# Performance work log

Measured on AMD Instinct MI355X. Metric: run time of the kernel, lower is better.

Reference implementation:

```python
import jax, jax.numpy as jnp
import numpy as np

L, B, T, C, H, FF = 2, 2, 2048, 512, 8, 1024
HS = C // H  # head size
EPS = 1.1920929e-07  # torch float32 finfo eps (nn.RMSNorm default)


def setup_inputs() -> dict:
    key = jax.random.key(0)
    ks = jax.random.split(key, 20)
    s = 0.02
    return {
        "hidden": jax.random.normal(ks[0], (B, T, C), jnp.float32),
        "target": jax.random.normal(ks[1], (B, T, C), jnp.float32),
        # self-attn per-head projections (bias=False)
        "Wq_s": jax.random.normal(ks[2], (L, H, C, HS)) * s,
        "Wk_s": jax.random.normal(ks[3], (L, H, C, HS)) * s,
        "Wv_s": jax.random.normal(ks[4], (L, H, C, HS)) * s,
        "Wo_s": jax.random.normal(ks[5], (L, C, C)) * s,
        "bo_s": jnp.zeros((L, C)),
        # cross-attn per-head projections
        "Wq_x": jax.random.normal(ks[6], (L, H, C, HS)) * s,
        "Wk_x": jax.random.normal(ks[7], (L, H, C, HS)) * s,
        "Wv_x": jax.random.normal(ks[8], (L, H, C, HS)) * s,
        "Wo_x": jax.random.normal(ks[9], (L, C, C)) * s,
        "bo_x": jnp.zeros((L, C)),
        # FFN
        "W1": jax.random.normal(ks[10], (L, C, FF)) * s,
        "b1": jnp.zeros((L, FF)),
        "W2": jax.random.normal(ks[11], (L, FF, C)) * s,
        "b2": jnp.zeros((L, C)),
        # RMSNorm gains ln1..ln4
        "g1": jnp.ones((L, C)),
        "g2": jnp.ones((L, C)),
        "g3": jnp.ones((L, C)),
        "g4": jnp.ones((L, C)),
    }


def _rms(x, g):
    return x * jax.lax.rsqrt(jnp.mean(x * x, axis=-1, keepdims=True) + EPS) * g


def _attn(q_in, kv_in, Wq, Wk, Wv, Wo, bo, causal):
    # q_in: [B,Tq,C], kv_in: [B,Tk,C]; W*: [H,C,HS]
    q = jnp.einsum('btc,hcd->bhtd', q_in, Wq)
    k = jnp.einsum('bsc,hcd->bhsd', kv_in, Wk)
    v = jnp.einsum('bsc,hcd->bhsd', kv_in, Wv)
    wei = jnp.einsum('bhtd,bhsd->bhts', q, k) * (HS ** -0.5)  # [B,H,Tq,Tk]
    if causal:
        Tq, Tk = q_in.shape[1], kv_in.shape[1]
        mask = jnp.tril(jnp.ones((Tq, Tk), bool))
        wei = jnp.where(mask, wei, -jnp.inf)
    wei = jax.nn.softmax(wei, axis=-1)
    out = jnp.einsum('bhts,bhsd->bhtd', wei, v)
    out = out.transpose(0, 2, 1, 3).reshape(q_in.shape[0], q_in.shape[1], C)
    return out @ Wo + bo


def reference(hidden, target, Wq_s, Wk_s, Wv_s, Wo_s, bo_s,
              Wq_x, Wk_x, Wv_x, Wo_x, bo_x,
              W1, b1, W2, b2, g1, g2, g3, g4):
    t = target
    for l in range(L):
        # masked self-attention with RMSNorm pre-norm + residual
        t = t + _attn(_rms(t, g1[l]), _rms(t, g1[l]), Wq_s[l], Wk_s[l], Wv_s[l],
                      Wo_s[l], bo_s[l], causal=True)
        # cross-attention: K/V from ln2(hidden), Q from ln3(t)
        t = t + _attn(_rms(t, g3[l]), _rms(hidden, g2[l]), Wq_x[l], Wk_x[l], Wv_x[l],
                      Wo_x[l], bo_x[l], causal=False)
        # GELU FFN
        h = _rms(t, g4[l])
        t = t + (jax.nn.gelu(h @ W1[l] + b1[l], approximate=False) @ W2[l] + b2[l])
    return t
```

## Files before the change

kernel.cpp:

```cpp
#include <hip/hip_runtime.h>
#include <hip/hip_bf16.h>
#include <math.h>

#define L 2
#define B 2
#define T 2048
#define C 512
#define H 8
#define FF 1024
#define HS 64
#define EPSV 1.1920929e-07f

typedef __hip_bfloat16 bf16;
typedef __attribute__((ext_vector_type(8))) short short8;
typedef __attribute__((ext_vector_type(4))) float f32x4;

__device__ __forceinline__ float b2f(bf16 x) { return __bfloat162float(x); }

__device__ __forceinline__ void gl16(const unsigned short* g, unsigned short* l) {
    __builtin_amdgcn_global_load_lds(
        (const __attribute__((address_space(1))) unsigned int*)g,
        (__attribute__((address_space(3))) unsigned int*)l, 16, 0, 0);
}

__global__ void detect_k(const unsigned short* __restrict__ g1bits, int* __restrict__ flag) {
    if (threadIdx.x == 0 && blockIdx.x == 0)
        *flag = (g1bits[0] != (unsigned short)0x3F80u) ? 1 : 0;
}

__device__ __forceinline__ float ld_in(const void* p, size_t i, int fl) {
    return fl ? ((const float*)p)[i] : b2f(((const bf16*)p)[i]);
}

#define QKVT_TOT 1572864
#define WO_TOT 524288
#define W12_TOT 1048576
#define SM_TOT 9216
#define ACT_TOT 2097152

struct TrArgs {
    const void *Wq_s, *Wk_s, *Wv_s, *Wq_x, *Wk_x, *Wv_x, *Wo_s, *Wo_x, *W1, *W2;
    bf16 *cQKVs, *cQKVx, *cWoTs, *cWoTx, *cW1T, *cW2T;
    const int* flag;
};

__global__ __launch_bounds__(256) void prep_tr_k(TrArgs a) {
    __shared__ float tile[32][33];
    int bid = blockIdx.x;
    int fl = *a.flag;
    const void* src; bf16* dst;
    size_t sbase;
    int srcLD, dstLD, r0, c0;
    if (bid < 3072) {
        int pid = bid >> 5, t = bid & 31;
        int which = pid / 48, rem = pid % 48;
        int l = rem / 24, rem2 = rem % 24;
        int p = rem2 >> 3, hh = rem2 & 7;
        src = which ? (p == 0 ? a.Wq_x : p == 1 ? a.Wk_x : a.Wv_x)
                    : (p == 0 ? a.Wq_s : p == 1 ? a.Wk_s : a.Wv_s);
        dst = (which ? a.cQKVx : a.cQKVs) + (size_t)l * 786432 + (size_t)(p * 512 + hh * 64) * 512;
        sbase = (size_t)(l * 8 + hh) * 32768;
        srcLD = 64; dstLD = 512;
        r0 = (t >> 1) * 32; c0 = (t & 1) * 32;
    } else if (bid < 4096) {
        int b2 = bid - 3072, pid = b2 >> 8, t = b2 & 255;
        int which = pid >> 1, l = pid & 1;
        src = which ? a.Wo_x : a.Wo_s;
        dst = (which ? a.cWoTx : a.cWoTs) + (size_t)l * 262144;
        sbase = (size_t)l * 262144;
        srcLD = 512; dstLD = 512;
        r0 = (t >> 4) * 32; c0 = (t & 15) * 32;
    } else if (bid < 5120) {
        int b2 = bid - 4096, l = b2 >> 9, t = b2 & 511;
        src = a.W1; dst = a.cW1T + (size_t)l * 524288; sbase = (size_t)l * 524288;
        srcLD = 1024; dstLD = 512;
        r0 = (t >> 5) * 32; c0 = (t & 31) * 32;
    } else {
        int b2 = bid - 5120, l = b2 >> 9, t = b2 & 511;
        src = a.W2; dst = a.cW2T + (size_t)l * 524288; sbase = (size_t)l * 524288;
        srcLD = 512; dstLD = 1024;
        r0 = (t >> 4) * 32; c0 = (t & 15) * 32;
    }
    int tx = threadIdx.x & 31, ty = threadIdx.x >> 5;
#pragma unroll
    for (int i = 0; i < 4; i++)
        tile[ty + i * 8][tx] = ld_in(src, sbase + (size_t)(r0 + ty + i * 8) * srcLD + c0 + tx, fl);
    __syncthreads();
#pragma unroll
    for (int i = 0; i < 4; i++)
        dst[(size_t)(c0 + ty + i * 8) * dstLD + r0 + tx] = __float2bfloat16(tile[tx][ty + i * 8]);
}

#define ACTQ 1048576
struct SmArgs {
    const void* sm[8];
    const void *hidden, *target;
    bf16* smallDst;
    float *hid, *t_buf;
    const int* flag;
};

__global__ void prep_small_k(SmArgs s) {
    int i = blockIdx.x * 256 + threadIdx.x;
    int fl = *s.flag;
    if (i < SM_TOT) {
        const int cum[9] = {0, 1024, 2048, 4096, 5120, 6144, 7168, 8192, 9216};
        int k = 0;
        while (i >= cum[k + 1]) k++;
        s.smallDst[i] = __float2bfloat16(ld_in(s.sm[k], i - cum[k], fl));
        return;
    }
    int q = i - SM_TOT;
    if (q >= ACTQ) return;
    int half = q >= (ACTQ / 2);
    size_t e = (size_t)(q - half * (ACTQ / 2)) * 4;
    const void* src = half ? s.target : s.hidden;
    float* dstf = half ? s.t_buf : s.hid;
    if (fl) {
        *(float4*)(dstf + e) = *(const float4*)((const float*)src + e);
    } else {
        ushort4 u = *(const ushort4*)((const unsigned short*)src + e);
        float4 v;
        v.x = __uint_as_float((unsigned)u.x << 16);
        v.y = __uint_as_float((unsigned)u.y << 16);
        v.z = __uint_as_float((unsigned)u.z << 16);
        v.w = __uint_as_float((unsigned)u.w << 16);
        *(float4*)(dstf + e) = v;
    }
}

__global__ void write_out_k(const float* __restrict__ in, void* __restrict__ out, int n,
                            const int* __restrict__ flag) {
    int i = blockIdx.x * blockDim.x + threadIdx.x;
    if (i >= n) return;
    if (*flag) ((float*)out)[i] = in[i];
    else       ((bf16*)out)[i] = __float2bfloat16(in[i]);
}

__global__ void rmsnorm_k(const float* __restrict__ x, const bf16* __restrict__ g,
                          bf16* __restrict__ y) {
    int row = blockIdx.x;
    int tid = threadIdx.x;
    const float* xr = x + (size_t)row * C;
    float v0 = xr[tid], v1 = xr[tid + 256];
    __shared__ float red[256];
    red[tid] = v0 * v0 + v1 * v1;
    __syncthreads();
    for (int s = 128; s > 0; s >>= 1) {
        if (tid < s) red[tid] += red[tid + s];
        __syncthreads();
    }
    float sc = rsqrtf(red[0] / (float)C + EPSV);
    y[(size_t)row * C + tid] = __float2bfloat16(v0 * sc * b2f(g[tid]));
    y[(size_t)row * C + tid + 256] = __float2bfloat16(v1 * sc * b2f(g[tid + 256]));
}

__global__ void rmsnorm2_k(const float* __restrict__ xa, const bf16* __restrict__ ga,
                           bf16* __restrict__ ya, const float* __restrict__ xb,
                           const bf16* __restrict__ gb, bf16* __restrict__ yb) {
    int sel = blockIdx.y;
    const float* x = sel ? xb : xa;
    const bf16* g = sel ? gb : ga;
    bf16* y = sel ? yb : ya;
    int row = blockIdx.x;
    int tid = threadIdx.x;
    const float* xr = x + (size_t)row * C;
    float v0 = xr[tid], v1 = xr[tid + 256];
    __shared__ float red[256];
    red[tid] = v0 * v0 + v1 * v1;
    __syncthreads();
    for (int s = 128; s > 0; s >>= 1) {
        if (tid < s) red[tid] += red[tid + s];
        __syncthreads();
    }
    float sc = rsqrtf(red[0] / (float)C + EPSV);
    y[(size_t)row * C + tid] = __float2bfloat16(v0 * sc * b2f(g[tid]));
    y[(size_t)row * C + tid + 256] = __float2bfloat16(v1 * sc * b2f(g[tid + 256]));
}

struct GDesc {
    const bf16* A; const bf16* Bt; const bf16* bias; float* resid; bf16* out;
    int N, K, ldOut, ep, nblkx, blkofs;
};
struct GBatch { GDesc d[3]; int nd; };

__global__ __launch_bounds__(256) void gemm64_k(GBatch gb) {
    int bid = blockIdx.x;
    int di = 0;
    if (gb.nd > 1 && bid >= gb.d[1].blkofs) di = 1;
    if (gb.nd > 2 && bid >= gb.d[2].blkofs) di = 2;
    GDesc g = gb.d[di];
    int lb = bid - g.blkofs;
    int bx = lb % g.nblkx, by = lb / g.nblkx;
    int m0 = by * 64, n0 = bx * 64;

    __shared__ alignas(16) unsigned short As[2][64 * 64];
    __shared__ alignas(16) unsigned short Bs[2][64 * 64];
    int tid = threadIdx.x, lane = tid & 63, wave = tid >> 6;
    int wr = wave >> 1, wc = wave & 1, quad = lane >> 4, l15 = lane & 15;
    const unsigned short* Au = (const unsigned short*)g.A;
    const unsigned short* Bu = (const unsigned short*)g.Bt;

    int r0 = tid >> 3, sg = tid & 7;
    int gs = sg ^ (r0 & 7);
    const unsigned short* agp0 = Au + (size_t)(m0 + r0) * g.K + gs * 8;
    const unsigned short* agp1 = Au + (size_t)(m0 + r0 + 32) * g.K + gs * 8;
    const unsigned short* bgp0 = Bu + (size_t)(n0 + r0) * g.K + gs * 8;
    const unsigned short* bgp1 = Bu + (size_t)(n0 + r0 + 32) * g.K + gs * 8;
    int wofs = wave * 512;

    f32x4 zf = {0.f, 0.f, 0.f, 0.f};
    f32x4 acc[2][2];
    acc[0][0] = zf; acc[0][1] = zf; acc[1][0] = zf; acc[1][1] = zf;

    int sws0 = ((quad) ^ (l15 & 7)) * 8;
    int sws1 = ((4 + quad) ^ (l15 & 7)) * 8;
    int arow = wr * 32 + l15, brow = wc * 32 + l15;

    int nk = g.K >> 6;
    {
        gl16(agp0, &As[0][wofs]);
        gl16(agp1, &As[0][wofs + 2048]);
        gl16(bgp0, &Bs[0][wofs]);
        gl16(bgp1, &Bs[0][wofs + 2048]);
    }
    int buf = 0;
    for (int kt = 0; kt < nk; kt++) {
        __builtin_amdgcn_sched_barrier(0);
        __builtin_amdgcn_s_barrier();
        __builtin_amdgcn_sched_barrier(0);
        if (kt + 1 < nk) {
            int ko = (kt + 1) << 6;
            gl16(agp0 + ko, &As[buf ^ 1][wofs]);
            gl16(agp1 + ko, &As[buf ^ 1][wofs + 2048]);
            gl16(bgp0 + ko, &Bs[buf ^ 1][wofs]);
            gl16(bgp1 + ko, &Bs[buf ^ 1][wofs + 2048]);
            asm volatile("s_waitcnt vmcnt(4)" ::: "memory");
        } else {
            asm volatile("s_waitcnt vmcnt(0)" ::: "memory");
        }
        __builtin_amdgcn_sched_barrier(0);
        __builtin_amdgcn_s_barrier();
        __builtin_amdgcn_sched_barrier(0);

        const unsigned short* Ab = As[buf];
        const unsigned short* Bb = Bs[buf];
        short8 a0[2], b0[2], a1[2], b1[2];
#pragma unroll
        for (int i = 0; i < 2; i++) {
            int ra = (arow + i * 16) << 6, rb = (brow + i * 16) << 6;
            a0[i] = *(const short8*)(Ab + ra + sws0);
            a1[i] = *(const short8*)(Ab + ra + sws1);
            b0[i] = *(const short8*)(Bb + rb + sws0);
            b1[i] = *(const short8*)(Bb + rb + sws1);
        }
#pragma unroll
        for (int mi = 0; mi < 2; mi++)
#pragma unroll
            for (int ni = 0; ni < 2; ni++) {
                acc[mi][ni] =
                    __builtin_amdgcn_mfma_f32_16x16x32_bf16(a0[mi], b0[ni], acc[mi][ni], 0, 0, 0);
                acc[mi][ni] =
                    __builtin_amdgcn_mfma_f32_16x16x32_bf16(a1[mi], b1[ni], acc[mi][ni], 0, 0, 0);
            }
        buf ^= 1;
    }

#pragma unroll
    for (int mi = 0; mi < 2; mi++) {
#pragma unroll
        for (int ni = 0; ni < 2; ni++) {
            int colg = n0 + wc * 32 + ni * 16 + l15;
            float bv = (g.ep == 1 || g.ep == 2) ? b2f(g.bias[colg]) : 0.f;
#pragma unroll
            for (int r2 = 0; r2 < 4; r2++) {
                int rowg = m0 + wr * 32 + mi * 16 + quad * 4 + r2;
                float v = acc[mi][ni][r2];
                if (g.ep == 0) {
                    g.out[(size_t)rowg * g.ldOut + colg] = __float2bfloat16(v);
                } else if (g.ep == 1) {
                    g.resid[(size_t)rowg * g.ldOut + colg] += v + bv;
                } else if (g.ep == 2) {
                    float u = v + bv;
                    g.out[(size_t)rowg * g.ldOut + colg] =
                        __float2bfloat16(0.5f * u * (1.f + erff(u * 0.70710678118654752f)));
                } else {
                    g.out[((size_t)((colg >> 11) * 512 + rowg) << 11) + (colg & 2047)] =
                        __float2bfloat16(v);
                }
            }
        }
    }
}

#define PST 72
__global__ __launch_bounds__(256) void attn_mfma_k(const bf16* __restrict__ qkv,
                                                   const bf16* __restrict__ vT,
                                                   bf16* __restrict__ attnout, int causal) {
    __shared__ alignas(16) unsigned short KsA[2][4096], VtA[2][4096];
    __shared__ unsigned short Ps[4][16 * PST];
    int qt = causal ? (gridDim.x - 1 - blockIdx.x) : blockIdx.x;
    int h = blockIdx.y, b = blockIdx.z;
    int tid = threadIdx.x, lane = tid & 63, w = tid >> 6;
    int quad = lane >> 4, l15 = lane & 15;
    const unsigned short* qk = (const unsigned short*)qkv;
    const unsigned short* vTp = (const unsigned short*)vT + ((size_t)b * 512 + h * 64) * T;
    size_t rowbase = (size_t)b * T;
    int koff = 512 + h * 64;
    unsigned short* Pw = Ps[w];
    bf16* Pwb = (bf16*)Pw;

    const unsigned short* qrow = qk + (rowbase + qt * 64 + w * 16 + l15) * 1536 + h * 64;
    short8 aq0 = *(const short8*)(qrow + quad * 8);
    short8 aq1 = *(const short8*)(qrow + 32 + quad * 8);

    int srow = lane >> 3;
    int ssp = (lane & 7) ^ (srow & 7);

    f32x4 zf = {0.f, 0.f, 0.f, 0.f};
    f32x4 oacc[4];
#pragma unroll
    for (int i = 0; i < 4; i++) oacc[i] = zf;
    float lpart[4] = {0.f, 0.f, 0.f, 0.f};

    int nT = causal ? (qt + 1) : (T / 64);

#pragma unroll
    for (int j = 0; j < 2; j++) {
        int c = w * 2 + j;
        int r = c * 8 + srow;
        gl16(qk + (rowbase + r) * 1536 + koff + ssp * 8, KsA[0] + c * 512);
        gl16(vTp + (size_t)r * T + ssp * 8, VtA[0] + c * 512);
    }
    __syncthreads();

    int buf = 0;
    for (int st = 0; st < nT; st++) {
        if (st + 1 < nT) {
#pragma unroll
            for (int j = 0; j < 2; j++) {
                int c = w * 2 + j;
                int r = c * 8 + srow;
                gl16(qk + (rowbase + (st + 1) * 64 + r) * 1536 + koff + ssp * 8,
                     KsA[buf ^ 1] + c * 512);
                gl16(vTp + (size_t)r * T + (st + 1) * 64 + ssp * 8, VtA[buf ^ 1] + c * 512);
            }
        }

        const unsigned short* Kb = KsA[buf];
        const unsigned short* Vb = VtA[buf];

        f32x4 sacc[4];
#pragma unroll
        for (int i = 0; i < 4; i++) sacc[i] = zf;
#pragma unroll
        for (int ni = 0; ni < 4; ni++) {
            int rr = ni * 16 + l15;
            short8 bk0 = *(const short8*)(Kb + rr * 64 + ((quad ^ (rr & 7)) * 8));
            short8 bk1 = *(const short8*)(Kb + rr * 64 + (((4 + quad) ^ (rr & 7)) * 8));
            sacc[ni] = __builtin_amdgcn_mfma_f32_16x16x32_bf16(aq0, bk0, sacc[ni], 0, 0, 0);
            sacc[ni] = __builtin_amdgcn_mfma_f32_16x16x32_bf16(aq1, bk1, sacc[ni], 0, 0, 0);
        }

        bool diag = causal && (st == qt);
        int qrl = w * 16 + quad * 4;
#pragma unroll
        for (int reg = 0; reg < 4; reg++) {
            float lp = 0.f;
#pragma unroll
            for (int ni = 0; ni < 4; ni++) {
                int s_l = ni * 16 + l15;
                float p = __expf(sacc[ni][reg] * 0.125f);
                if (diag && s_l > qrl + reg) p = 0.f;
                lp += p;
                Pwb[(quad * 4 + reg) * PST + s_l] = __float2bfloat16(p);
            }
            lpart[reg] += lp;
        }

        short8 ap0 = *(const short8*)(Pw + l15 * PST + quad * 8);
        short8 ap1 = *(const short8*)(Pw + l15 * PST + 32 + quad * 8);
#pragma unroll
        for (int dj = 0; dj < 4; dj++) {
            int rr = dj * 16 + l15;
            short8 bv0 = *(const short8*)(Vb + rr * 64 + ((quad ^ (rr & 7)) * 8));
            short8 bv1 = *(const short8*)(Vb + rr * 64 + (((4 + quad) ^ (rr & 7)) * 8));
            oacc[dj] = __builtin_amdgcn_mfma_f32_16x16x32_bf16(ap0, bv0, oacc[dj], 0, 0, 0);
            oacc[dj] = __builtin_amdgcn_mfma_f32_16x16x32_bf16(ap1, bv1, oacc[dj], 0, 0, 0);
        }

        __syncthreads();
        buf ^= 1;
    }

#pragma unroll
    for (int reg = 0; reg < 4; reg++) {
#pragma unroll
        for (int mk = 1; mk < 16; mk <<= 1) lpart[reg] += __shfl_xor(lpart[reg], mk, 64);
        lpart[reg] = 1.0f / lpart[reg];
    }
#pragma unroll
    for (int dj = 0; dj < 4; dj++) {
        int d = dj * 16 + l15;
#pragma unroll
        for (int reg = 0; reg < 4; reg++) {
            int q = w * 16 + quad * 4 + reg;
            attnout[(rowbase + qt * 64 + q) * C + h * HS + d] =
                __float2bfloat16(oacc[dj][reg] * lpart[reg]);
        }
    }
}

extern "C" void kernel_launch(void* const* d_in, const int* in_sizes, int n_in,
                              void* d_out, int out_size, void* d_ws, size_t ws_size,
                              hipStream_t stream) {
    const int BTC = B * T * C;
    const int BTF = B * T * FF;

    char* wsb = (char*)d_ws;
    int* flag = (int*)wsb;
    bf16* cur = (bf16*)(wsb + 256);
    bf16* cQKVs = cur;   cur += QKVT_TOT;
    bf16* cQKVx = cur;   cur += QKVT_TOT;
    bf16* cWoTs = cur;   cur += WO_TOT;
    bf16* cWoTx = cur;   cur += WO_TOT;
    bf16* cW1T = cur;    cur += W12_TOT;
    bf16* cW2T = cur;    cur += W12_TOT;
    bf16* smallBase = cur;
    bf16* cbo_s = cur;   cur += L * C;
    bf16* cbo_x = cur;   cur += L * C;
    bf16* cb1 = cur;     cur += L * FF;
    bf16* cb2 = cur;     cur += L * C;
    bf16* cg1 = cur;     cur += L * C;
    bf16* cg2 = cur;     cur += L * C;
    bf16* cg3 = cur;     cur += L * C;
    bf16* cg4 = cur;     cur += L * C;
    bf16* n1 = cur;      cur += BTC;
    bf16* n2 = cur;      cur += BTC;
    bf16* qkvbuf = cur;  cur += B * T * 3 * C;
    bf16* vTbuf = cur;   cur += BTC;
    bf16* attnout = cur; cur += BTC;
    bf16* h1buf = cur;   cur += BTF;
    size_t f32_off = (((char*)cur - wsb) + 255) & ~(size_t)255;
    float* t_buf = (float*)(wsb + f32_off);
    float* hid = t_buf + BTC;

    dim3 blk256(256);
    detect_k<<<1, 64, 0, stream>>>((const unsigned short*)d_in[16], flag);

    TrArgs ta;
    ta.Wq_s = d_in[2]; ta.Wk_s = d_in[3]; ta.Wv_s = d_in[4];
    ta.Wq_x = d_in[7]; ta.Wk_x = d_in[8]; ta.Wv_x = d_in[9];
    ta.Wo_s = d_in[5]; ta.Wo_x = d_in[10]; ta.W1 = d_in[12]; ta.W2 = d_in[14];
    ta.cQKVs = cQKVs; ta.cQKVx = cQKVx; ta.cWoTs = cWoTs; ta.cWoTx = cWoTx;
    ta.cW1T = cW1T; ta.cW2T = cW2T; ta.flag = flag;
    prep_tr_k<<<6144, blk256, 0, stream>>>(ta);

    SmArgs sa;
    sa.sm[0] = d_in[6];  sa.sm[1] = d_in[11]; sa.sm[2] = d_in[13]; sa.sm[3] = d_in[15];
    sa.sm[4] = d_in[16]; sa.sm[5] = d_in[17]; sa.sm[6] = d_in[18]; sa.sm[7] = d_in[19];
    sa.hidden = d_in[0]; sa.target = d_in[1];
    sa.smallDst = smallBase; sa.hid = hid; sa.t_buf = t_buf; sa.flag = flag;
    prep_small_k<<<(SM_TOT + ACTQ + 255) / 256, blk256, 0, stream>>>(sa);

    const int M = B * T;
    dim3 attngrid(T / 64, H, B);

    for (int l = 0; l < L; l++) {
        bf16* qkvW_s = cQKVs + (size_t)l * 3 * C * C;
        bf16* qkvW_x = cQKVx + (size_t)l * 3 * C * C;
        bf16* woT_s = cWoTs + (size_t)l * C * C;
        bf16* woT_x = cWoTx + (size_t)l * C * C;
        bf16* w1T = cW1T + (size_t)l * C * FF;
        bf16* w2T = cW2T + (size_t)l * FF * C;

        rmsnorm_k<<<M, blk256, 0, stream>>>(t_buf, cg1 + l * C, n1);
        {
            GBatch gb;
            gb.nd = 2;
            gb.d[0] = {n1, qkvW_s, nullptr, nullptr, qkvbuf, 1024, C, 3 * C, 0, 16, 0};
            gb.d[1] = {qkvW_s + (size_t)1024 * C, n1, nullptr, nullptr, vTbuf,
                       M, C, 0, 3, 64, 1024};
            gemm64_k<<<1024 + 512, blk256, 0, stream>>>(gb);
        }
        attn_mfma_k<<<attngrid, blk256, 0, stream>>>(qkvbuf, vTbuf, attnout, 1);
        {
            GBatch gb;
            gb.nd = 1;
            gb.d[0] = {attnout, woT_s, cbo_s + l * C, t_buf, nullptr, C, C, C, 1, 8, 0};
            gemm64_k<<<512, blk256, 0, stream>>>(gb);
        }

        rmsnorm2_k<<<dim3(M, 2), blk256, 0, stream>>>(t_buf, cg3 + l * C, n1, hid, cg2 + l * C, n2);
        {
            GBatch gb;
            gb.nd = 3;
            gb.d[0] = {n1, qkvW_x, nullptr, nullptr, qkvbuf, C, C, 3 * C, 0, 8, 0};
            gb.d[1] = {n2, qkvW_x + (size_t)512 * C, nullptr, nullptr, qkvbuf + C,
                       C, C, 3 * C, 0, 8, 512};
            gb.d[2] = {qkvW_x + (size_t)1024 * C, n2, nullptr, nullptr, vTbuf,
                       M, C, 0, 3, 64, 1024};
            gemm64_k<<<512 + 512 + 512, blk256, 0, stream>>>(gb);
        }
        attn_mfma_k<<<attngrid, blk256, 0, stream>>>(qkvbuf, vTbuf, attnout, 0);
        {
            GBatch gb;
            gb.nd = 1;
            gb.d[0] = {attnout, woT_x, cbo_x + l * C, t_buf, nullptr, C, C, C, 1, 8, 0};
            gemm64_k<<<512, blk256, 0, stream>>>(gb);
        }

        rmsnorm_k<<<M, blk256, 0, stream>>>(t_buf, cg4 + l * C, n1);
        {
            GBatch gb;
            gb.nd = 1;
            gb.d[0] = {n1, w1T, cb1 + l * FF, nullptr, h1buf, FF, C, FF, 2, 16, 0};
            gemm64_k<<<1024, blk256, 0, stream>>>(gb);
        }
        {
            GBatch gb;
            gb.nd = 1;
            gb.d[0] = {h1buf, w2T, cb2 + l * C, t_buf, nullptr, C, FF, C, 1, 8, 0};
            gemm64_k<<<512, blk256, 0, stream>>>(gb);
        }
    }

    write_out_k<<<(BTC + 255) / 256, blk256, 0, stream>>>(t_buf, d_out, BTC, flag);
}
```

Before: 512.6 us.

## Split-K residual GEMMs with atomics, wave-shuffle RMSNorm reduction, MFMA priority hints

The output-projection and FFN-down GEMMs, which add into the fp32 residual, are split along K into two halves. This doubles the block count from 512 to 1024, and each half accumulates into the residual with atomicAdd. RMSNorm reductions now use wave-level shuffles plus a 4-entry shared array instead of a tree reduction with many barriers. The attention kernel raises wave priority around its MFMA loops. Atomic float adds make the summation order nondeterministic and add atomic traffic in exchange for better occupancy on the small-N GEMMs.

```diff
diff --git a/kernel.cpp b/kernel.cpp
--- a/kernel.cpp
+++ b/kernel.cpp
@@ -143,14 +143,13 @@
     int tid = threadIdx.x;
     const float* xr = x + (size_t)row * C;
     float v0 = xr[tid], v1 = xr[tid + 256];
-    __shared__ float red[256];
-    red[tid] = v0 * v0 + v1 * v1;
+    float s = v0 * v0 + v1 * v1;
+#pragma unroll
+    for (int mk = 1; mk < 64; mk <<= 1) s += __shfl_xor(s, mk, 64);
+    __shared__ float ws[4];
+    if ((tid & 63) == 0) ws[tid >> 6] = s;
     __syncthreads();
-    for (int s = 128; s > 0; s >>= 1) {
-        if (tid < s) red[tid] += red[tid + s];
-        __syncthreads();
-    }
-    float sc = rsqrtf(red[0] / (float)C + EPSV);
+    float sc = rsqrtf((ws[0] + ws[1] + ws[2] + ws[3]) / (float)C + EPSV);
     y[(size_t)row * C + tid] = __float2bfloat16(v0 * sc * b2f(g[tid]));
     y[(size_t)row * C + tid + 256] = __float2bfloat16(v1 * sc * b2f(g[tid + 256]));
 }
@@ -166,21 +165,20 @@
     int tid = threadIdx.x;
     const float* xr = x + (size_t)row * C;
     float v0 = xr[tid], v1 = xr[tid + 256];
-    __shared__ float red[256];
-    red[tid] = v0 * v0 + v1 * v1;
+    float s = v0 * v0 + v1 * v1;
+#pragma unroll
+    for (int mk = 1; mk < 64; mk <<= 1) s += __shfl_xor(s, mk, 64);
+    __shared__ float ws[4];
+    if ((tid & 63) == 0) ws[tid >> 6] = s;
     __syncthreads();
-    for (int s = 128; s > 0; s >>= 1) {
-        if (tid < s) red[tid] += red[tid + s];
-        __syncthreads();
-    }
-    float sc = rsqrtf(red[0] / (float)C + EPSV);
+    float sc = rsqrtf((ws[0] + ws[1] + ws[2] + ws[3]) / (float)C + EPSV);
     y[(size_t)row * C + tid] = __float2bfloat16(v0 * sc * b2f(g[tid]));
     y[(size_t)row * C + tid + 256] = __float2bfloat16(v1 * sc * b2f(g[tid + 256]));
 }
 
 struct GDesc {
     const bf16* A; const bf16* Bt; const bf16* bias; float* resid; bf16* out;
-    int N, K, ldOut, ep, nblkx, blkofs;
+    int N, K, ldOut, ep, nblkx, blkofs, ldAB, kofs;
 };
 struct GBatch { GDesc d[3]; int nd; };
 
@@ -203,10 +201,10 @@
 
     int r0 = tid >> 3, sg = tid & 7;
     int gs = sg ^ (r0 & 7);
-    const unsigned short* agp0 = Au + (size_t)(m0 + r0) * g.K + gs * 8;
-    const unsigned short* agp1 = Au + (size_t)(m0 + r0 + 32) * g.K + gs * 8;
-    const unsigned short* bgp0 = Bu + (size_t)(n0 + r0) * g.K + gs * 8;
-    const unsigned short* bgp1 = Bu + (size_t)(n0 + r0 + 32) * g.K + gs * 8;
+    const unsigned short* agp0 = Au + (size_t)(m0 + r0) * g.ldAB + g.kofs + gs * 8;
+    const unsigned short* agp1 = Au + (size_t)(m0 + r0 + 32) * g.ldAB + g.kofs + gs * 8;
+    const unsigned short* bgp0 = Bu + (size_t)(n0 + r0) * g.ldAB + g.kofs + gs * 8;
+    const unsigned short* bgp1 = Bu + (size_t)(n0 + r0 + 32) * g.ldAB + g.kofs + gs * 8;
     int wofs = wave * 512;
 
     f32x4 zf = {0.f, 0.f, 0.f, 0.f};
@@ -271,7 +269,7 @@
 #pragma unroll
         for (int ni = 0; ni < 2; ni++) {
             int colg = n0 + wc * 32 + ni * 16 + l15;
-            float bv = (g.ep == 1 || g.ep == 2) ? b2f(g.bias[colg]) : 0.f;
+            float bv = (g.bias && (g.ep == 1 || g.ep == 2)) ? b2f(g.bias[colg]) : 0.f;
 #pragma unroll
             for (int r2 = 0; r2 < 4; r2++) {
                 int rowg = m0 + wr * 32 + mi * 16 + quad * 4 + r2;
@@ -279,7 +277,7 @@
                 if (g.ep == 0) {
                     g.out[(size_t)rowg * g.ldOut + colg] = __float2bfloat16(v);
                 } else if (g.ep == 1) {
-                    g.resid[(size_t)rowg * g.ldOut + colg] += v + bv;
+                    atomicAdd(&g.resid[(size_t)rowg * g.ldOut + colg], v + bv);
                 } else if (g.ep == 2) {
                     float u = v + bv;
                     g.out[(size_t)rowg * g.ldOut + colg] =
@@ -353,6 +351,7 @@
         f32x4 sacc[4];
 #pragma unroll
         for (int i = 0; i < 4; i++) sacc[i] = zf;
+        __builtin_amdgcn_s_setprio(1);
 #pragma unroll
         for (int ni = 0; ni < 4; ni++) {
             int rr = ni * 16 + l15;
@@ -361,6 +360,7 @@
             sacc[ni] = __builtin_amdgcn_mfma_f32_16x16x32_bf16(aq0, bk0, sacc[ni], 0, 0, 0);
             sacc[ni] = __builtin_amdgcn_mfma_f32_16x16x32_bf16(aq1, bk1, sacc[ni], 0, 0, 0);
         }
+        __builtin_amdgcn_s_setprio(0);
 
         bool diag = causal && (st == qt);
         int qrl = w * 16 + quad * 4;
@@ -380,6 +380,7 @@
 
         short8 ap0 = *(const short8*)(Pw + l15 * PST + quad * 8);
         short8 ap1 = *(const short8*)(Pw + l15 * PST + 32 + quad * 8);
+        __builtin_amdgcn_s_setprio(1);
 #pragma unroll
         for (int dj = 0; dj < 4; dj++) {
             int rr = dj * 16 + l15;
@@ -388,6 +389,7 @@
             oacc[dj] = __builtin_amdgcn_mfma_f32_16x16x32_bf16(ap0, bv0, oacc[dj], 0, 0, 0);
             oacc[dj] = __builtin_amdgcn_mfma_f32_16x16x32_bf16(ap1, bv1, oacc[dj], 0, 0, 0);
         }
+        __builtin_amdgcn_s_setprio(0);
 
         __syncthreads();
         buf ^= 1;
@@ -478,50 +480,53 @@
         {
             GBatch gb;
             gb.nd = 2;
-            gb.d[0] = {n1, qkvW_s, nullptr, nullptr, qkvbuf, 1024, C, 3 * C, 0, 16, 0};
+            gb.d[0] = {n1, qkvW_s, nullptr, nullptr, qkvbuf, 1024, C, 3 * C, 0, 16, 0, C, 0};
             gb.d[1] = {qkvW_s + (size_t)1024 * C, n1, nullptr, nullptr, vTbuf,
-                       M, C, 0, 3, 64, 1024};
+                       M, C, 0, 3, 64, 1024, C, 0};
             gemm64_k<<<1024 + 512, blk256, 0, stream>>>(gb);
         }
         attn_mfma_k<<<attngrid, blk256, 0, stream>>>(qkvbuf, vTbuf, attnout, 1);
         {
             GBatch gb;
-            gb.nd = 1;
-            gb.d[0] = {attnout, woT_s, cbo_s + l * C, t_buf, nullptr, C, C, C, 1, 8, 0};
-            gemm64_k<<<512, blk256, 0, stream>>>(gb);
+            gb.nd = 2;
+            gb.d[0] = {attnout, woT_s, cbo_s + l * C, t_buf, nullptr, C, 256, C, 1, 8, 0, C, 0};
+            gb.d[1] = {attnout, woT_s, nullptr, t_buf, nullptr, C, 256, C, 1, 8, 512, C, 256};
+            gemm64_k<<<1024, blk256, 0, stream>>>(gb);
         }
 
         rmsnorm2_k<<<dim3(M, 2), blk256, 0, stream>>>(t_buf, cg3 + l * C, n1, hid, cg2 + l * C, n2);
         {
             GBatch gb;
             gb.nd = 3;
-            gb.d[0] = {n1, qkvW_x, nullptr, nullptr, qkvbuf, C, C, 3 * C, 0, 8, 0};
+            gb.d[0] = {n1, qkvW_x, nullptr, nullptr, qkvbuf, C, C, 3 * C, 0, 8, 0, C, 0};
             gb.d[1] = {n2, qkvW_x + (size_t)512 * C, nullptr, nullptr, qkvbuf + C,
-                       C, C, 3 * C, 0, 8, 512};
+                       C, C, 3 * C, 0, 8, 512, C, 0};
             gb.d[2] = {qkvW_x + (size_t)1024 * C, n2, nullptr, nullptr, vTbuf,
-                       M, C, 0, 3, 64, 1024};
+                       M, C, 0, 3, 64, 1024, C, 0};
             gemm64_k<<<512 + 512 + 512, blk256, 0, stream>>>(gb);
         }
         attn_mfma_k<<<attngrid, blk256, 0, stream>>>(qkvbuf, vTbuf, attnout, 0);
         {
             GBatch gb;
-            gb.nd = 1;
-            gb.d[0] = {attnout, woT_x, cbo_x + l * C, t_buf, nullptr, C, C, C, 1, 8, 0};
-            gemm64_k<<<512, blk256, 0, stream>>>(gb);
+            gb.nd = 2;
+            gb.d[0] = {attnout, woT_x, cbo_x + l * C, t_buf, nullptr, C, 256, C, 1, 8, 0, C, 0};
+            gb.d[1] = {attnout, woT_x, nullptr, t_buf, nullptr, C, 256, C, 1, 8, 512, C, 256};
+            gemm64_k<<<1024, blk256, 0, stream>>>(gb);
         }
 
         rmsnorm_k<<<M, blk256, 0, stream>>>(t_buf, cg4 + l * C, n1);
         {
             GBatch gb;
             gb.nd = 1;
-            gb.d[0] = {n1, w1T, cb1 + l * FF, nullptr, h1buf, FF, C, FF, 2, 16, 0};
+            gb.d[0] = {n1, w1T, cb1 + l * FF, nullptr, h1buf, FF, C, FF, 2, 16, 0, C, 0};
             gemm64_k<<<1024, blk256, 0, stream>>>(gb);
         }
         {
             GBatch gb;
-            gb.nd = 1;
-            gb.d[0] = {h1buf, w2T, cb2 + l * C, t_buf, nullptr, C, FF, C, 1, 8, 0};
-            gemm64_k<<<512, blk256, 0, stream>>>(gb);
+            gb.nd = 2;
+            gb.d[0] = {h1buf, w2T, cb2 + l * C, t_buf, nullptr, C, 512, C, 1, 8, 0, FF, 0};
+            gb.d[1] = {h1buf, w2T, nullptr, t_buf, nullptr, C, 512, C, 1, 8, 512, FF, 512};
+            gemm64_k<<<1024, blk256, 0, stream>>>(gb);
         }
     }
 
```

Result: slower. 538.3 us (+5.0%).
